# Kernel tuning notes

Measured on AMD Instinct MI355X. Metric: run time of the kernel, lower is better.

The kernel has to match this reference:

```python
import jax, jax.numpy as jnp
import numpy as np

D_STATE = 8
DT_RANK = 16
D_CONV = 4


def layernorm(x, w, b, eps=1e-5):
    mu = jnp.mean(x, axis=-1, keepdims=True)
    var = jnp.var(x, axis=-1, keepdims=True)
    return (x - mu) * jax.lax.rsqrt(var + eps) * w + b


def silu(x):
    return x * jax.nn.sigmoid(x)


def dwconv_causal(x, w, b):
    # x: [B,L,D], w: [D,K] depthwise causal conv (mamba conv1d, padding=K-1 then truncate)
    K = w.shape[1]
    xp = jnp.pad(x, ((0, 0), (K - 1, 0), (0, 0)))
    y = jax.lax.conv_general_dilated(
        xp, w.T[:, None, :], (1,), 'VALID',
        dimension_numbers=('NWC', 'WIO', 'NWC'),
        feature_group_count=w.shape[0])
    return y + b


def selective_scan(u, dt, A, Bm, Cm, Dp):
    # u, dt: [b,l,d]; A: [d,n]; Bm, Cm: [b,l,n]; Dp: [d]
    def step(h, inp):
        dt_t, B_t, C_t, u_t = inp           # [b,d],[b,n],[b,n],[b,d]
        dA = jnp.exp(dt_t[..., None] * A)   # [b,d,n]
        h = dA * h + dt_t[..., None] * B_t[:, None, :] * u_t[..., None]
        y = jnp.einsum('bdn,bn->bd', h, C_t)
        return h, y
    b, l, d = u.shape
    h0 = jnp.zeros((b, d, A.shape[1]), u.dtype)
    xs = (dt.transpose(1, 0, 2), Bm.transpose(1, 0, 2),
          Cm.transpose(1, 0, 2), u.transpose(1, 0, 2))
    _, ys = jax.lax.scan(step, h0, xs)
    return ys.transpose(1, 0, 2) + u * Dp


def scan_dir(x, xe, cw, cb, cew, ceb, xpw, dtw, dtb, A_log, Dp):
    # one scan direction: u from x (input0 path), dt/B/C from xe (extra_emb path)
    xc = silu(dwconv_causal(x, cw, cb))
    ec = silu(dwconv_causal(xe, cew, ceb))
    dbl = ec @ xpw.T                                   # [b,l,dt_rank+2n]
    dtr = dbl[..., :DT_RANK]
    Bm = dbl[..., DT_RANK:DT_RANK + D_STATE]
    Cm = dbl[..., DT_RANK + D_STATE:]
    dt = jax.nn.softplus(dtr @ dtw.T + dtb)
    A = -jnp.exp(A_log)
    return selective_scan(xc, dt, A, Bm, Cm, Dp)


def forward(input0, input1, norm0_w, norm0_b, norm1_w, norm1_b,
            in_proj_w, in_proj_extra_w,
            convx_w, convx_b, conve_w, conve_b,
            convx_w_r, convx_b_r, conve_w_r, conve_b_r,
            xproj_w, xproj_w_r, dtproj_w, dtproj_b, dtproj_w_r, dtproj_b_r,
            A_log, A_log_r, Dp, Dp_r, outnorm_w, outnorm_b, outproj_w):
    skip = input0
    h0 = layernorm(input0, norm0_w, norm0_b)
    h1 = layernorm(input1, norm1_w, norm1_b)
    xz = h0 @ in_proj_w.T                     # [b,l,2d]
    d = in_proj_w.shape[0] // 2
    x, z = xz[..., :d], xz[..., d:]
    xe = h1 @ in_proj_extra_w.T               # [b,l,d]
    # forward-direction scan
    y_f = scan_dir(x, xe, convx_w, convx_b, conve_w, conve_b,
                   xproj_w, dtproj_w, dtproj_b, A_log, Dp)
    # backward-direction scan (flip sequence, scan, flip back)
    xr, xer = jnp.flip(x, 1), jnp.flip(xe, 1)
    y_b = scan_dir(xr, xer, convx_w_r, convx_b_r, conve_w_r, conve_b_r,
                   xproj_w_r, dtproj_w_r, dtproj_b_r, A_log_r, Dp_r)
    y = (y_f + jnp.flip(y_b, 1)) * 0.5        # if_devide_out=True
    y = layernorm(y, outnorm_w, outnorm_b)    # use_norm=True
    y = y * silu(z)
    out = y @ outproj_w.T
    return out + skip


def setup_inputs() -> dict:
    key = jax.random.key(0)
    B, H, W, dim = 2, 128, 128, 256
    L, d, n, dtr, K = H * W, dim, D_STATE, DT_RANK, D_CONV
    ks = jax.random.split(key, 24)
    s = 0.02
    inp = {
        'input0': jax.random.normal(ks[0], (B, L, dim), jnp.float32),
        'input1': jax.random.normal(ks[1], (B, L, dim), jnp.float32),
        'norm0_w': jnp.ones((dim,), jnp.float32),
        'norm0_b': jnp.zeros((dim,), jnp.float32),
        'norm1_w': jnp.ones((dim,), jnp.float32),
        'norm1_b': jnp.zeros((dim,), jnp.float32),
        'in_proj_w': jax.random.normal(ks[2], (2 * d, dim), jnp.float32) * s,
        'in_proj_extra_w': jax.random.normal(ks[3], (d, dim), jnp.float32) * s,
        'convx_w': jax.random.normal(ks[4], (d, K), jnp.float32) * 0.2,
        'convx_b': jnp.zeros((d,), jnp.float32),
        'conve_w': jax.random.normal(ks[5], (d, K), jnp.float32) * 0.2,
        'conve_b': jnp.zeros((d,), jnp.float32),
        'convx_w_r': jax.random.normal(ks[6], (d, K), jnp.float32) * 0.2,
        'convx_b_r': jnp.zeros((d,), jnp.float32),
        'conve_w_r': jax.random.normal(ks[7], (d, K), jnp.float32) * 0.2,
        'conve_b_r': jnp.zeros((d,), jnp.float32),
        'xproj_w': jax.random.normal(ks[8], (dtr + 2 * n, d), jnp.float32) * s,
        'xproj_w_r': jax.random.normal(ks[9], (dtr + 2 * n, d), jnp.float32) * s,
        'dtproj_w': jax.random.normal(ks[10], (d, dtr), jnp.float32) * 0.1,
        'dtproj_b': jax.random.uniform(ks[11], (d,), jnp.float32, -4.0, -2.0),
        'dtproj_w_r': jax.random.normal(ks[12], (d, dtr), jnp.float32) * 0.1,
        'dtproj_b_r': jax.random.uniform(ks[13], (d,), jnp.float32, -4.0, -2.0),
        'A_log': jnp.tile(jnp.log(jnp.arange(1, n + 1, dtype=jnp.float32)), (d, 1)),
        'A_log_r': jnp.tile(jnp.log(jnp.arange(1, n + 1, dtype=jnp.float32)), (d, 1)),
        'Dp': jnp.ones((d,), jnp.float32),
        'Dp_r': jnp.ones((d,), jnp.float32),
        'outnorm_w': jnp.ones((d,), jnp.float32),
        'outnorm_b': jnp.zeros((d,), jnp.float32),
        'outproj_w': jax.random.normal(ks[14], (dim, d), jnp.float32) * s,
    }
    return inp


def reference(input0, input1, norm0_w, norm0_b, norm1_w, norm1_b,
              in_proj_w, in_proj_extra_w,
              convx_w, convx_b, conve_w, conve_b,
              convx_w_r, convx_b_r, conve_w_r, conve_b_r,
              xproj_w, xproj_w_r, dtproj_w, dtproj_b, dtproj_w_r, dtproj_b_r,
              A_log, A_log_r, Dp, Dp_r, outnorm_w, outnorm_b, outproj_w):
    return forward(input0, input1, norm0_w, norm0_b, norm1_w, norm1_b,
                   in_proj_w, in_proj_extra_w,
                   convx_w, convx_b, conve_w, conve_b,
                   convx_w_r, convx_b_r, conve_w_r, conve_b_r,
                   xproj_w, xproj_w_r, dtproj_w, dtproj_b, dtproj_w_r, dtproj_b_r,
                   A_log, A_log_r, Dp, Dp_r, outnorm_w, outnorm_b, outproj_w)
```

## Files before the change

### kernel.cpp

```cpp
#include <hip/hip_runtime.h>
#include <math.h>

#define L_SEQ 16384
#define DIM 256
#define NST 8
#define RNK 16
#define S_TOT 32768
#define NCH 512
#define CLH 32

typedef __attribute__((ext_vector_type(8))) short bf16x8;
typedef __attribute__((ext_vector_type(4))) float f32x4;

__device__ __forceinline__ float bf2f(unsigned short u) {
  union { unsigned int i; float f; } v; v.i = ((unsigned int)u) << 16; return v.f;
}
__device__ __forceinline__ unsigned short f2bf(float x) {
  union { float f; unsigned int i; } v; v.f = x;
  unsigned int r = v.i + 0x7fffu + ((v.i >> 16) & 1u);
  return (unsigned short)(r >> 16);
}
__device__ __forceinline__ float rcpf(float x) {
  return __builtin_amdgcn_rcpf(x);
}

__global__ __launch_bounds__(256) void wconv(
    const float* __restrict__ w0, const float* __restrict__ w1,
    const float* __restrict__ w2, unsigned short* __restrict__ out) {
  int i = blockIdx.x * 256 + threadIdx.x;
  if (i < 131072) out[i] = f2bf(w0[i]);
  else if (i < 196608) out[i] = f2bf(w1[i - 131072]);
  else out[i] = f2bf(w2[i - 196608]);
}

__global__ __launch_bounds__(256) void ln_norm(
    const float* __restrict__ in0, const float* __restrict__ in1,
    const float* __restrict__ w0, const float* __restrict__ b0,
    const float* __restrict__ w1, const float* __restrict__ b1,
    unsigned short* __restrict__ h0, unsigned short* __restrict__ h1) {
  int which = blockIdx.y;
  int row = blockIdx.x * 4 + (threadIdx.x >> 6);
  int lane = threadIdx.x & 63;
  const float* x = (which ? in1 : in0) + (size_t)row * DIM;
  const float* w = which ? w1 : w0;
  const float* b = which ? b1 : b0;
  unsigned short* h = which ? h1 : h0;
  float4 v = *(const float4*)&x[lane * 4];
  float s = v.x + v.y + v.z + v.w;
  float s2 = v.x * v.x + v.y * v.y + v.z * v.z + v.w * v.w;
  for (int off = 32; off; off >>= 1) {
    s += __shfl_xor(s, off);
    s2 += __shfl_xor(s2, off);
  }
  float mean = s * (1.0f / DIM);
  float var = s2 * (1.0f / DIM) - mean * mean;
  float rstd = rsqrtf(var + 1e-5f);
  float4 wv = *(const float4*)&w[lane * 4];
  float4 bv = *(const float4*)&b[lane * 4];
  ushort4 out;
  out.x = f2bf((v.x - mean) * rstd * wv.x + bv.x);
  out.y = f2bf((v.y - mean) * rstd * wv.y + bv.y);
  out.z = f2bf((v.z - mean) * rstd * wv.z + bv.z);
  out.w = f2bf((v.w - mean) * rstd * wv.w + bv.w);
  *(ushort4*)&h[(size_t)row * DIM + lane * 4] = out;
}

template <int BF16C, int ADDIN>
__global__ __launch_bounds__(256) void gemm64(
    const unsigned short* __restrict__ A, int lda,
    const unsigned short* __restrict__ Wb,
    void* __restrict__ Cv, const float* __restrict__ addp, int Nn) {
  __shared__ unsigned short As[64 * 256];
  __shared__ unsigned short Ws[64 * 256];
  int tid = threadIdx.x;
  int n0 = blockIdx.x * 64, m0 = blockIdx.y * 64;
  for (int i = 0; i < 8; ++i) {
    int f8 = tid + i * 256;
    int r = f8 >> 5, c8 = (f8 & 31) * 8;
    int sc = c8 ^ ((r & 7) << 3);
    *(uint4*)&As[r * 256 + sc] = *(const uint4*)&A[(size_t)(m0 + r) * lda + c8];
    *(uint4*)&Ws[r * 256 + sc] = *(const uint4*)&Wb[(size_t)(n0 + r) * 256 + c8];
  }
  __syncthreads();
  int wid = tid >> 6, lane = tid & 63;
  int wm = wid >> 1, wn = wid & 1;
  int l15 = lane & 15, lk = (lane >> 4) * 8;
  f32x4 acc[2][2] = {};
  for (int ks = 0; ks < 8; ++ks) {
    int kcol = ks * 32 + lk;
    bf16x8 af[2], bf_[2];
    for (int mf = 0; mf < 2; ++mf) {
      int row = wm * 32 + mf * 16 + l15;
      af[mf] = *(const bf16x8*)&As[row * 256 + (kcol ^ ((row & 7) << 3))];
    }
    for (int nf = 0; nf < 2; ++nf) {
      int row = wn * 32 + nf * 16 + l15;
      bf_[nf] = *(const bf16x8*)&Ws[row * 256 + (kcol ^ ((row & 7) << 3))];
    }
    for (int mf = 0; mf < 2; ++mf)
      for (int nf = 0; nf < 2; ++nf)
        acc[mf][nf] = __builtin_amdgcn_mfma_f32_16x16x32_bf16(
            af[mf], bf_[nf], acc[mf][nf], 0, 0, 0);
  }
  for (int mf = 0; mf < 2; ++mf)
    for (int nf = 0; nf < 2; ++nf) {
      int row = m0 + wm * 32 + mf * 16 + (lane >> 4) * 4;
      int col = n0 + wn * 32 + nf * 16 + l15;
      for (int v = 0; v < 4; ++v) {
        size_t off = (size_t)(row + v) * Nn + col;
        float val = acc[mf][nf][v];
        if (ADDIN) val += addp[off];
        if (BF16C) ((unsigned short*)Cv)[off] = f2bf(val);
        else       ((float*)Cv)[off] = val;
      }
    }
}

__global__ __launch_bounds__(256) void xproj_mfma(
    const unsigned short* __restrict__ xe,
    const float* __restrict__ conve_w, const float* __restrict__ conve_b,
    const float* __restrict__ conve_w_r, const float* __restrict__ conve_b_r,
    const float* __restrict__ xproj_w, const float* __restrict__ xproj_w_r,
    float* __restrict__ dbl2) {
  __shared__ unsigned short ecS[64 * 256];
  __shared__ unsigned short xwS[32 * 256];
  int chunk = blockIdx.x;
  int dir = blockIdx.y;
  int b = chunk >> 8;
  int t0 = (chunk & 255) * 64;
  int tid = threadIdx.x;
  const float* cw = dir ? conve_w_r : conve_w;
  const float* cb = dir ? conve_b_r : conve_b;
  const float* xw = dir ? xproj_w_r : xproj_w;

  for (int i = tid; i < 32 * 256; i += 256) {
    int o = i >> 8, dd = i & 255;
    xwS[o * 256 + (((dd & ~7) ^ ((o & 7) << 3)) | (dd & 7))] = f2bf(xw[i]);
  }

  {
    int c = tid;
    float w0 = cw[c * 4 + 0], w1 = cw[c * 4 + 1], w2 = cw[c * 4 + 2],
          w3 = cw[c * 4 + 3], bias = cb[c];
    size_t bL = (size_t)b * L_SEQ;
    auto loadx = [&](int t) -> float {
      if (t < 0) return 0.f;
      int src = dir ? (L_SEQ - 1 - t) : t;
      return bf2f(xe[(bL + src) * DIM + c]);
    };
    float xm3 = loadx(t0 - 3), xm2 = loadx(t0 - 2), xm1 = loadx(t0 - 1);
    const unsigned short* xp =
        &xe[(bL + (dir ? (L_SEQ - 1 - t0) : t0)) * DIM + c];
    int xstep = dir ? -DIM : DIM;
    int cbase = c & ~7, clow = c & 7;
    for (int t4 = 0; t4 < 64; t4 += 4) {
      float xin4[4];
      for (int j = 0; j < 4; ++j) xin4[j] = bf2f(xp[(ptrdiff_t)j * xstep]);
      xp += (ptrdiff_t)4 * xstep;
      for (int j = 0; j < 4; ++j) {
        int tl = t4 + j;
        float xin = xin4[j];
        float pre = w0 * xm3 + w1 * xm2 + w2 * xm1 + w3 * xin + bias;
        float u = pre * rcpf(1.f + __expf(-pre));
        xm3 = xm2; xm2 = xm1; xm1 = xin;
        ecS[tl * 256 + ((cbase ^ ((tl & 7) << 3)) | clow)] = f2bf(u);
      }
    }
  }
  __syncthreads();

  int wid = tid >> 6, lane = tid & 63;
  int l15 = lane & 15, lk = (lane >> 4) * 8;
  f32x4 acc[2] = {};
  for (int kk = 0; kk < 8; ++kk) {
    int kcol = kk * 32 + lk;
    int row = wid * 16 + l15;
    bf16x8 af = *(const bf16x8*)&ecS[row * 256 + (kcol ^ ((row & 7) << 3))];
    for (int ni = 0; ni < 2; ++ni) {
      int o = ni * 16 + l15;
      bf16x8 bfr = *(const bf16x8*)&xwS[o * 256 + (kcol ^ ((o & 7) << 3))];
      acc[ni] = __builtin_amdgcn_mfma_f32_16x16x32_bf16(af, bfr, acc[ni], 0, 0, 0);
    }
  }
  size_t mbase = (size_t)dir * S_TOT + (size_t)chunk * 64;
  int rloc = wid * 16 + (lane >> 4) * 4;
  for (int ni = 0; ni < 2; ++ni) {
    int o = ni * 16 + l15;
    for (int v = 0; v < 4; ++v)
      dbl2[(mbase + rloc + v) * 32 + o] = acc[ni][v];
  }
}

__global__ __launch_bounds__(256) void dt_mfma(
    const float* __restrict__ dbl2,
    const float* __restrict__ dtw, const float* __restrict__ dtw_r,
    const float* __restrict__ dtb, const float* __restrict__ dtb_r,
    unsigned short* __restrict__ dt_arr) {
  __shared__ unsigned short dtwS[256 * 32];
  __shared__ unsigned short dtrS[64 * 32];
  __shared__ unsigned short outS[64 * 256];
  int m0 = blockIdx.x * 64;
  int dir = (blockIdx.x >= 512) ? 1 : 0;
  int tid = threadIdx.x;
  const float* dw = dir ? dtw_r : dtw;
  const float* db = dir ? dtb_r : dtb;
  {
    uint4 z; z.x = 0; z.y = 0; z.z = 0; z.w = 0;
    for (int i = tid; i < 1280; i += 256) {
      if (i < 1024) ((uint4*)dtwS)[i] = z;
      else          ((uint4*)dtrS)[i - 1024] = z;
    }
  }
  __syncthreads();
  for (int it = 0; it < 4; ++it) {
    int idx = tid + it * 256;
    int c = idx >> 2, k4 = idx & 3;
    float4 v = *(const float4*)&dw[c * 16 + k4 * 4];
    uint2 pk;
    pk.x = (unsigned int)f2bf(v.x) | ((unsigned int)f2bf(v.y) << 16);
    pk.y = (unsigned int)f2bf(v.z) | ((unsigned int)f2bf(v.w) << 16);
    int byte = c * 64 + (((k4 >> 1) ^ (c & 3)) << 4) + ((k4 & 1) << 3);
    *(uint2*)((char*)dtwS + byte) = pk;
  }
  {
    int r = tid >> 2, k4 = tid & 3;
    float4 v = *(const float4*)&dbl2[(size_t)(m0 + r) * 32 + k4 * 4];
    uint2 pk;
    pk.x = (unsigned int)f2bf(v.x) | ((unsigned int)f2bf(v.y) << 16);
    pk.y = (unsigned int)f2bf(v.z) | ((unsigned int)f2bf(v.w) << 16);
    int byte = r * 64 + (((k4 >> 1) ^ (r & 3)) << 4) + ((k4 & 1) << 3);
    *(uint2*)((char*)dtrS + byte) = pk;
  }
  __syncthreads();
  int wid = tid >> 6, lane = tid & 63;
  int l15 = lane & 15, lkc = lane >> 4;
  bf16x8 af[4];
  for (int mi = 0; mi < 4; ++mi) {
    int r = mi * 16 + l15;
    af[mi] = *(const bf16x8*)((char*)dtrS + r * 64 + ((lkc ^ (r & 3)) << 4));
  }
  f32x4 acc[4][4] = {};
  for (int ni = 0; ni < 4; ++ni) {
    int c = (wid * 4 + ni) * 16 + l15;
    bf16x8 bfr = *(const bf16x8*)((char*)dtwS + c * 64 + ((lkc ^ (c & 3)) << 4));
    for (int mi = 0; mi < 4; ++mi)
      acc[mi][ni] = __builtin_amdgcn_mfma_f32_16x16x32_bf16(
          af[mi], bfr, acc[mi][ni], 0, 0, 0);
  }
  for (int ni = 0; ni < 4; ++ni) {
    int c = (wid * 4 + ni) * 16 + l15;
    float bias_ = db[c];
    int cb_ = c & ~7, cl_ = c & 7;
    for (int mi = 0; mi < 4; ++mi) {
      int rb = mi * 16 + (lane >> 4) * 4;
      for (int v = 0; v < 4; ++v) {
        int r = rb + v;
        float xdt = acc[mi][ni][v] + bias_;
        float dtv = (xdt > 15.f) ? xdt : __logf(1.f + __expf(xdt));
        outS[r * 256 + ((cb_ ^ ((r & 7) << 3)) | cl_)] = f2bf(dtv);
      }
    }
  }
  __syncthreads();
  for (int it = 0; it < 8; ++it) {
    int i = tid + it * 256;
    int r = i >> 5, cg = (i & 31) * 8;
    uint4 val = *(const uint4*)&outS[r * 256 + (cg ^ ((r & 7) << 3))];
    *(uint4*)&dt_arr[(size_t)(m0 + r) * 256 + cg] = val;
  }
}

__global__ __launch_bounds__(256) void u_compute(
    const unsigned short* __restrict__ xz,
    const float* __restrict__ convx_w, const float* __restrict__ convx_b,
    const float* __restrict__ convx_w_r, const float* __restrict__ convx_b_r,
    unsigned short* __restrict__ u_arr) {
  int chunk = blockIdx.x;
  int dir = blockIdx.y;
  int b = chunk >> 9;
  int t0 = (chunk & 511) * 32;
  int c = threadIdx.x;
  const float* cw = dir ? convx_w_r : convx_w;
  const float* cb = dir ? convx_b_r : convx_b;
  float w0 = cw[c * 4 + 0], w1 = cw[c * 4 + 1], w2 = cw[c * 4 + 2],
        w3 = cw[c * 4 + 3], bias = cb[c];
  size_t dtbase = (size_t)dir * S_TOT + (size_t)b * L_SEQ;
  size_t bL = (size_t)b * L_SEQ;
  float xm3, xm2, xm1;
  {
    auto loadx = [&](int t) -> float {
      if (t < 0) return 0.f;
      int src = dir ? (L_SEQ - 1 - t) : t;
      return bf2f(xz[(bL + src) * 512 + c]);
    };
    xm3 = loadx(t0 - 3); xm2 = loadx(t0 - 2); xm1 = loadx(t0 - 1);
  }
  const unsigned short* xp = &xz[(bL + (dir ? (L_SEQ - 1 - t0) : t0)) * 512 + c];
  ptrdiff_t xstep = dir ? -512 : 512;
  unsigned short* op = &u_arr[(dtbase + t0) * DIM + c];
  for (int t4 = 0; t4 < 32; t4 += 4) {
    float xin4[4];
    for (int j = 0; j < 4; ++j) xin4[j] = bf2f(xp[(ptrdiff_t)j * xstep]);
    xp += 4 * xstep;
    for (int j = 0; j < 4; ++j) {
      float xin = xin4[j];
      float pre = w0 * xm3 + w1 * xm2 + w2 * xm1 + w3 * xin + bias;
      float u = pre * rcpf(1.f + __expf(-pre));
      xm3 = xm2; xm2 = xm1; xm1 = xin;
      op[(size_t)j * DIM] = f2bf(u);
    }
    op += 4 * DIM;
  }
}

#define DA8(FASTA)                                                    \
  float dA[NST];                                                      \
  if (FASTA) {                                                        \
    float e1 = __expf(-dtv);                                          \
    dA[0] = e1;                                                       \
    for (int n = 1; n < NST; ++n) dA[n] = dA[n - 1] * e1;             \
  } else {                                                            \
    for (int n = 0; n < NST; ++n) dA[n] = __expf(dtv * Ar[n]);        \
  }

template <int USE_UDT>
__global__ __launch_bounds__(256) void scan_pass1(
    const unsigned short* __restrict__ xz, const float* __restrict__ dbl2,
    const unsigned short* __restrict__ u_arr,
    const unsigned short* __restrict__ dt_arr,
    const float* __restrict__ convx_w, const float* __restrict__ convx_b,
    const float* __restrict__ convx_w_r, const float* __restrict__ convx_b_r,
    const float* __restrict__ dtproj_w, const float* __restrict__ dtproj_b,
    const float* __restrict__ dtproj_w_r, const float* __restrict__ dtproj_b_r,
    const float* __restrict__ A_log, const float* __restrict__ A_log_r,
    float* __restrict__ Pc, float* __restrict__ Qc) {
  int chunk = blockIdx.x, b = blockIdx.y, dir = blockIdx.z;
  int d = threadIdx.x;
  const float* al = dir ? A_log_r : A_log;
  float w0 = 0.f, w1 = 0.f, w2 = 0.f, w3 = 0.f, bias = 0.f, dbias = 0.f;
  float dwreg[RNK];
  if (!USE_UDT) {
    const float* cw = dir ? convx_w_r : convx_w;
    const float* cb = dir ? convx_b_r : convx_b;
    const float* dw = dir ? dtproj_w_r : dtproj_w;
    const float* dbp = dir ? dtproj_b_r : dtproj_b;
    w0 = cw[d * 4 + 0]; w1 = cw[d * 4 + 1]; w2 = cw[d * 4 + 2];
    w3 = cw[d * 4 + 3]; bias = cb[d]; dbias = dbp[d];
    for (int r = 0; r < RNK; ++r) dwreg[r] = dw[d * RNK + r];
  }
  float Ar[NST];
  bool fa = true;
  for (int n = 0; n < NST; ++n) {
    Ar[n] = -__expf(al[d * NST + n]);
    fa = fa && (fabsf(Ar[n] + (float)(n + 1)) < 1e-4f * (float)(n + 1));
  }
  bool fastA = (__ballot(fa) == ~0ULL);

  __shared__ float dblS[CLH][32];
  int t0 = chunk * CLH;
  size_t dtbase = (size_t)dir * S_TOT + (size_t)b * L_SEQ;
  if (USE_UDT) {
    int i = d;
    dblS[i >> 3][i & 7] = dbl2[(dtbase + t0 + (i >> 3)) * 32 + 16 + (i & 7)];
  } else {
    for (int i = d; i < CLH * 32; i += 256)
      dblS[i >> 5][i & 31] = dbl2[(dtbase + t0) * 32 + i];
  }
  __syncthreads();
  auto loadx = [&](int t) -> float {
    if (t < 0) return 0.f;
    int srct = dir ? (L_SEQ - 1 - t) : t;
    return bf2f(xz[((size_t)b * L_SEQ + srct) * 512 + d]);
  };
  float xm3 = 0.f, xm2 = 0.f, xm1 = 0.f;
  if (!USE_UDT) { xm3 = loadx(t0 - 3); xm2 = loadx(t0 - 2); xm1 = loadx(t0 - 1); }
  const unsigned short* up = &u_arr[(dtbase + t0) * DIM + d];
  const unsigned short* dtp = &dt_arr[(dtbase + t0) * DIM + d];
  float Q[NST];
  for (int n = 0; n < NST; ++n) Q[n] = 0.f;
  float sdt = 0.f;
  const int BOFF = USE_UDT ? 0 : 16;

#define P1_GRP(FASTA)                                                      \
  for (int t8 = 0; t8 < CLH; t8 += 8) {                                    \
    float uu[8], dd[8];                                                    \
    for (int j = 0; j < 8; ++j) {                                          \
      uu[j] = bf2f(up[(size_t)j * DIM]);                                   \
      dd[j] = bf2f(dtp[(size_t)j * DIM]);                                  \
    }                                                                      \
    up += 8 * DIM; dtp += 8 * DIM;                                         \
    for (int j = 0; j < 8; ++j) {                                          \
      const float* row = dblS[t8 + j];                                     \
      float u = uu[j], dtv = dd[j];                                        \
      float du = dtv * u;                                                  \
      sdt += dtv;                                                          \
      DA8(FASTA)                                                           \
      float4 B0 = *(const float4*)(row);                                   \
      float4 B1 = *(const float4*)(row + 4);                               \
      Q[0] = dA[0] * Q[0] + du * B0.x; Q[1] = dA[1] * Q[1] + du * B0.y;    \
      Q[2] = dA[2] * Q[2] + du * B0.z; Q[3] = dA[3] * Q[3] + du * B0.w;    \
      Q[4] = dA[4] * Q[4] + du * B1.x; Q[5] = dA[5] * Q[5] + du * B1.y;    \
      Q[6] = dA[6] * Q[6] + du * B1.z; Q[7] = dA[7] * Q[7] + du * B1.w;    \
    }                                                                      \
  }

#define P1_STEP(FASTA)                                                     \
  {                                                                        \
    const float* row = dblS[tl];                                           \
    float u, dtv;                                                          \
    {                                                                      \
      float xin = loadx(t0 + tl);                                          \
      float pre = w0 * xm3 + w1 * xm2 + w2 * xm1 + w3 * xin + bias;        \
      u = pre * rcpf(1.f + __expf(-pre));                                  \
      xm3 = xm2; xm2 = xm1; xm1 = xin;                                     \
      float4 q0 = *(const float4*)(row);                                   \
      float4 q1 = *(const float4*)(row + 4);                               \
      float4 q2 = *(const float4*)(row + 8);                               \
      float4 q3 = *(const float4*)(row + 12);                              \
      float xdt = dbias + q0.x * dwreg[0] + q0.y * dwreg[1] +              \
                  q0.z * dwreg[2] + q0.w * dwreg[3] + q1.x * dwreg[4] +    \
                  q1.y * dwreg[5] + q1.z * dwreg[6] + q1.w * dwreg[7] +    \
                  q2.x * dwreg[8] + q2.y * dwreg[9] + q2.z * dwreg[10] +   \
                  q2.w * dwreg[11] + q3.x * dwreg[12] + q3.y * dwreg[13] + \
                  q3.z * dwreg[14] + q3.w * dwreg[15];                     \
      dtv = (xdt > 15.f) ? xdt : __logf(1.f + __expf(xdt));                \
    }                                                                      \
    float du = dtv * u;                                                    \
    sdt += dtv;                                                            \
    DA8(FASTA)                                                             \
    float4 B0 = *(const float4*)(row + BOFF);                              \
    float4 B1 = *(const float4*)(row + BOFF + 4);                          \
    Q[0] = dA[0] * Q[0] + du * B0.x; Q[1] = dA[1] * Q[1] + du * B0.y;      \
    Q[2] = dA[2] * Q[2] + du * B0.z; Q[3] = dA[3] * Q[3] + du * B0.w;      \
    Q[4] = dA[4] * Q[4] + du * B1.x; Q[5] = dA[5] * Q[5] + du * B1.y;      \
    Q[6] = dA[6] * Q[6] + du * B1.z; Q[7] = dA[7] * Q[7] + du * B1.w;      \
  }

  if (USE_UDT) {
    if (fastA) { P1_GRP(1) } else { P1_GRP(0) }
  } else {
    if (fastA) {
      for (int tl = 0; tl < CLH; ++tl) P1_STEP(1)
    } else {
      for (int tl = 0; tl < CLH; ++tl) P1_STEP(0)
    }
  }
#undef P1_STEP
#undef P1_GRP

  float P[NST];
  if (fastA) {
    float E = __expf(-sdt);
    P[0] = E;
    for (int n = 1; n < NST; ++n) P[n] = P[n - 1] * E;
  } else {
    for (int n = 0; n < NST; ++n) P[n] = __expf(Ar[n] * sdt);
  }
  size_t obase = ((((size_t)(dir * 2 + b)) * NCH + chunk) * DIM + d) * NST;
  for (int n = 0; n < NST; ++n) { Pc[obase + n] = P[n]; Qc[obase + n] = Q[n]; }
}

__global__ __launch_bounds__(256) void scan_mid(
    float* __restrict__ Pc, const float* __restrict__ Qc) {
  int idx = blockIdx.x * 256 + threadIdx.x;
  int dn = idx & 2047;
  int db_ = idx >> 11;
  size_t base = (size_t)db_ * NCH * 2048 + dn;
  float h = 0.f;
  for (int c0 = 0; c0 < NCH; c0 += 8) {
    size_t off = base + (size_t)c0 * 2048;
    float P[8], Q[8];
#pragma unroll
    for (int j = 0; j < 8; ++j) {
      P[j] = Pc[off + (size_t)j * 2048];
      Q[j] = Qc[off + (size_t)j * 2048];
    }
#pragma unroll
    for (int j = 0; j < 8; ++j) {
      Pc[off + (size_t)j * 2048] = h;
      h = P[j] * h + Q[j];
    }
  }
}

template <int MODE>
__global__ __launch_bounds__(256) void scan_pass2(
    const unsigned short* __restrict__ xz, const float* __restrict__ dbl2,
    unsigned short* __restrict__ u_arr,
    const unsigned short* __restrict__ dt_arr,
    const float* __restrict__ convx_w, const float* __restrict__ convx_b,
    const float* __restrict__ convx_w_r, const float* __restrict__ convx_b_r,
    const float* __restrict__ dtproj_w, const float* __restrict__ dtproj_b,
    const float* __restrict__ dtproj_w_r, const float* __restrict__ dtproj_b_r,
    const float* __restrict__ A_log, const float* __restrict__ A_log_r,
    const float* __restrict__ Dp, const float* __restrict__ Dp_r,
    const float* __restrict__ Hinit, unsigned short* __restrict__ ycomb,
    int dirParam) {
  int chunk = blockIdx.x, b = blockIdx.y;
  int dir = MODE ? blockIdx.z : dirParam;
  int d = threadIdx.x;
  const float* al = dir ? A_log_r : A_log;
  float Dv = (dir ? Dp_r : Dp)[d];
  float w0 = 0.f, w1 = 0.f, w2 = 0.f, w3 = 0.f, bias = 0.f, dbias = 0.f;
  float dwreg[RNK];
  if (!MODE) {
    const float* cw = dir ? convx_w_r : convx_w;
    const float* cb = dir ? convx_b_r : convx_b;
    const float* dw = dir ? dtproj_w_r : dtproj_w;
    const float* dbp = dir ? dtproj_b_r : dtproj_b;
    w0 = cw[d * 4 + 0]; w1 = cw[d * 4 + 1]; w2 = cw[d * 4 + 2];
    w3 = cw[d * 4 + 3]; bias = cb[d];
    dbias = dbp[d];
    for (int r = 0; r < RNK; ++r) dwreg[r] = dw[d * RNK + r];
  }
  float Ar[NST];
  bool fa = true;
  for (int n = 0; n < NST; ++n) {
    Ar[n] = -__expf(al[d * NST + n]);
    fa = fa && (fabsf(Ar[n] + (float)(n + 1)) < 1e-4f * (float)(n + 1));
  }
  bool fastA = (__ballot(fa) == ~0ULL);

  __shared__ float dblS[CLH][32];
  int t0 = chunk * CLH;
  size_t dtbase = (size_t)dir * S_TOT + (size_t)b * L_SEQ;
  if (MODE) {
    for (int i = d; i < CLH * 16; i += 256)
      dblS[i >> 4][i & 15] = dbl2[(dtbase + t0 + (i >> 4)) * 32 + 16 + (i & 15)];
  } else {
    for (int i = d; i < CLH * 32; i += 256)
      dblS[i >> 5][i & 31] = dbl2[(dtbase + t0) * 32 + i];
  }
  __syncthreads();
  auto loadx = [&](int t) -> float {
    if (t < 0) return 0.f;
    int srct = dir ? (L_SEQ - 1 - t) : t;
    return bf2f(xz[((size_t)b * L_SEQ + srct) * 512 + d]);
  };
  float xm3 = 0.f, xm2 = 0.f, xm1 = 0.f;
  if (!MODE) { xm3 = loadx(t0 - 3); xm2 = loadx(t0 - 2); xm1 = loadx(t0 - 1); }
  float h[NST];
  size_t hbase = ((((size_t)(dir * 2 + b)) * NCH + chunk) * DIM + d) * NST;
  for (int n = 0; n < NST; ++n) h[n] = Hinit[hbase + n];
  unsigned short* up = &u_arr[(dtbase + t0) * DIM + d];
  const unsigned short* dtp = &dt_arr[(dtbase + t0) * DIM + d];
  unsigned short* yc = &ycomb[((size_t)b * L_SEQ + t0) * DIM + d];

#define P2_GRP(FASTA)                                                      \
  for (int t8 = 0; t8 < CLH; t8 += 8) {                                    \
    float uu[8], dd[8];                                                    \
    for (int j = 0; j < 8; ++j) {                                          \
      uu[j] = bf2f(up[(size_t)j * DIM]);                                   \
      dd[j] = bf2f(dtp[(size_t)j * DIM]);                                  \
    }                                                                      \
    for (int j = 0; j < 8; ++j) {                                          \
      const float* row = dblS[t8 + j];                                     \
      float u = uu[j], dtv = dd[j];                                        \
      float du = dtv * u;                                                  \
      DA8(FASTA)                                                           \
      float4 B0 = *(const float4*)(row);                                   \
      float4 B1 = *(const float4*)(row + 4);                               \
      float4 C0 = *(const float4*)(row + 8);                               \
      float4 C1 = *(const float4*)(row + 12);                              \
      h[0] = dA[0] * h[0] + du * B0.x; h[1] = dA[1] * h[1] + du * B0.y;    \
      h[2] = dA[2] * h[2] + du * B0.z; h[3] = dA[3] * h[3] + du * B0.w;    \
      h[4] = dA[4] * h[4] + du * B1.x; h[5] = dA[5] * h[5] + du * B1.y;    \
      h[6] = dA[6] * h[6] + du * B1.z; h[7] = dA[7] * h[7] + du * B1.w;    \
      float y = C0.x * h[0] + C0.y * h[1] + C0.z * h[2] + C0.w * h[3] +    \
                C1.x * h[4] + C1.y * h[5] + C1.z * h[6] + C1.w * h[7] +    \
                u * Dv;                                                    \
      if (dir == 0) yc[(size_t)j * DIM] = f2bf(y);                         \
      else          up[(size_t)j * DIM] = f2bf(y);                         \
    }                                                                      \
    up += 8 * DIM; dtp += 8 * DIM; yc += 8 * DIM;                          \
  }

#define P2_STEP(FASTA)                                                     \
  {                                                                        \
    int t = t0 + tl;                                                       \
    const float* row = dblS[tl];                                           \
    float u, dtv;                                                          \
    {                                                                      \
      float xin = loadx(t);                                                \
      float pre = w0 * xm3 + w1 * xm2 + w2 * xm1 + w3 * xin + bias;        \
      u = pre * rcpf(1.f + __expf(-pre));                                  \
      xm3 = xm2; xm2 = xm1; xm1 = xin;                                     \
      float4 q0 = *(const float4*)(row);                                   \
      float4 q1 = *(const float4*)(row + 4);                               \
      float4 q2 = *(const float4*)(row + 8);                               \
      float4 q3 = *(const float4*)(row + 12);                              \
      float xdt = dbias + q0.x * dwreg[0] + q0.y * dwreg[1] +              \
                  q0.z * dwreg[2] + q0.w * dwreg[3] + q1.x * dwreg[4] +    \
                  q1.y * dwreg[5] + q1.z * dwreg[6] + q1.w * dwreg[7] +    \
                  q2.x * dwreg[8] + q2.y * dwreg[9] + q2.z * dwreg[10] +   \
                  q2.w * dwreg[11] + q3.x * dwreg[12] + q3.y * dwreg[13] + \
                  q3.z * dwreg[14] + q3.w * dwreg[15];                     \
      dtv = (xdt > 15.f) ? xdt : __logf(1.f + __expf(xdt));                \
    }                                                                      \
    float du = dtv * u;                                                    \
    DA8(FASTA)                                                             \
    float4 B0 = *(const float4*)(row + 16);                                \
    float4 B1 = *(const float4*)(row + 20);                                \
    float4 C0 = *(const float4*)(row + 24);                                \
    float4 C1 = *(const float4*)(row + 28);                                \
    h[0] = dA[0] * h[0] + du * B0.x; h[1] = dA[1] * h[1] + du * B0.y;      \
    h[2] = dA[2] * h[2] + du * B0.z; h[3] = dA[3] * h[3] + du * B0.w;      \
    h[4] = dA[4] * h[4] + du * B1.x; h[5] = dA[5] * h[5] + du * B1.y;      \
    h[6] = dA[6] * h[6] + du * B1.z; h[7] = dA[7] * h[7] + du * B1.w;      \
    float y = C0.x * h[0] + C0.y * h[1] + C0.z * h[2] + C0.w * h[3] +      \
              C1.x * h[4] + C1.y * h[5] + C1.z * h[6] + C1.w * h[7] +      \
              u * Dv;                                                      \
    if (dir == 0) {                                                        \
      ycomb[((size_t)b * L_SEQ + t) * DIM + d] = f2bf(y);                  \
    } else {                                                               \
      size_t o = ((size_t)b * L_SEQ + (L_SEQ - 1 - t)) * DIM + d;          \
      float prev = bf2f(ycomb[o]);                                         \
      ycomb[o] = f2bf(0.5f * (prev + y));                                  \
    }                                                                      \
  }

  if (MODE) {
    if (fastA) { P2_GRP(1) } else { P2_GRP(0) }
  } else {
    if (fastA) {
      for (int tl = 0; tl < CLH; ++tl) P2_STEP(1)
    } else {
      for (int tl = 0; tl < CLH; ++tl) P2_STEP(0)
    }
  }
#undef P2_STEP
#undef P2_GRP
}

template <int MERGED>
__global__ __launch_bounds__(256) void combine_ln(
    const unsigned short* __restrict__ ycomb,
    const unsigned short* __restrict__ ybu,
    unsigned short* __restrict__ xz,
    const float* __restrict__ onw, const float* __restrict__ onb) {
  int m = blockIdx.x * 4 + (threadIdx.x >> 6);
  int lane = threadIdx.x & 63;
  ushort4 y4 = *(const ushort4*)&ycomb[(size_t)m * DIM + lane * 4];
  float v0 = bf2f(y4.x), v1 = bf2f(y4.y), v2 = bf2f(y4.z), v3 = bf2f(y4.w);
  if (MERGED) {
    int b = m >> 14, l = m & (L_SEQ - 1);
    size_t fo = ((size_t)S_TOT + (size_t)b * L_SEQ + (L_SEQ - 1 - l)) * DIM +
                lane * 4;
    ushort4 yb4 = *(const ushort4*)&ybu[fo];
    v0 = 0.5f * (v0 + bf2f(yb4.x)); v1 = 0.5f * (v1 + bf2f(yb4.y));
    v2 = 0.5f * (v2 + bf2f(yb4.z)); v3 = 0.5f * (v3 + bf2f(yb4.w));
  }
  float s = v0 + v1 + v2 + v3;
  float s2 = v0 * v0 + v1 * v1 + v2 * v2 + v3 * v3;
  for (int off = 32; off; off >>= 1) {
    s += __shfl_xor(s, off);
    s2 += __shfl_xor(s2, off);
  }
  float mean = s * (1.0f / DIM);
  float var = s2 * (1.0f / DIM) - mean * mean;
  float rstd = rsqrtf(var + 1e-5f);
  ushort4 z4 = *(const ushort4*)&xz[(size_t)m * 512 + 256 + lane * 4];
  float zf[4] = {bf2f(z4.x), bf2f(z4.y), bf2f(z4.z), bf2f(z4.w)};
  float vf[4] = {v0, v1, v2, v3};
  ushort4 out;
  unsigned short* op = (unsigned short*)&out;
  for (int j = 0; j < 4; ++j) {
    int c = lane * 4 + j;
    float ln = (vf[j] - mean) * rstd * onw[c] + onb[c];
    op[j] = f2bf(ln * (zf[j] * rcpf(1.f + __expf(-zf[j]))));
  }
  *(ushort4*)&xz[(size_t)m * 512 + lane * 4] = out;
}

extern "C" void kernel_launch(void* const* d_in, const int* in_sizes, int n_in,
                              void* d_out, int out_size, void* d_ws, size_t ws_size,
                              hipStream_t stream) {
  const float* input0 = (const float*)d_in[0];
  const float* input1 = (const float*)d_in[1];
  const float* norm0_w = (const float*)d_in[2];
  const float* norm0_b = (const float*)d_in[3];
  const float* norm1_w = (const float*)d_in[4];
  const float* norm1_b = (const float*)d_in[5];
  const float* in_proj_w = (const float*)d_in[6];
  const float* in_proj_extra_w = (const float*)d_in[7];
  const float* convx_w = (const float*)d_in[8];
  const float* convx_b = (const float*)d_in[9];
  const float* conve_w = (const float*)d_in[10];
  const float* conve_b = (const float*)d_in[11];
  const float* convx_w_r = (const float*)d_in[12];
  const float* convx_b_r = (const float*)d_in[13];
  const float* conve_w_r = (const float*)d_in[14];
  const float* conve_b_r = (const float*)d_in[15];
  const float* xproj_w = (const float*)d_in[16];
  const float* xproj_w_r = (const float*)d_in[17];
  const float* dtproj_w = (const float*)d_in[18];
  const float* dtproj_b = (const float*)d_in[19];
  const float* dtproj_w_r = (const float*)d_in[20];
  const float* dtproj_b_r = (const float*)d_in[21];
  const float* A_log = (const float*)d_in[22];
  const float* A_log_r = (const float*)d_in[23];
  const float* Dp = (const float*)d_in[24];
  const float* Dp_r = (const float*)d_in[25];
  const float* outnorm_w = (const float*)d_in[26];
  const float* outnorm_b = (const float*)d_in[27];
  const float* outproj_w = (const float*)d_in[28];

  char* w = (char*)d_ws;
  unsigned short* xz    = (unsigned short*)(w + 0);
  unsigned short* h1    = (unsigned short*)(w + 0);
  unsigned short* h0    = (unsigned short*)(w + 33554432);
  unsigned short* ycomb = (unsigned short*)(w + 33554432);
  float* Qc   = (float*)(w + 33554432);
  unsigned short* xe    = (unsigned short*)(w + 50331648);
  float* Pc   = (float*)(w + 50331648);
  float* dbl2 = (float*)(w + 67108864);
  unsigned short* wb = (unsigned short*)(w + 75497472);
  unsigned short* wb_in  = wb;
  unsigned short* wb_ex  = wb + 131072;
  unsigned short* wb_out = wb + 196608;
  unsigned short* u_arr  = (unsigned short*)(w + 76021760);
  unsigned short* dt_arr = (unsigned short*)(w + 109576192);
  const bool big = ws_size >= 76021760ULL + 67108864ULL;

  wconv<<<dim3(1024), 256, 0, stream>>>(in_proj_w, in_proj_extra_w, outproj_w, wb);
  ln_norm<<<dim3(S_TOT / 4, 2), 256, 0, stream>>>(
      input0, input1, norm0_w, norm0_b, norm1_w, norm1_b, h0, h1);
  gemm64<1, 0><<<dim3(4, 512), 256, 0, stream>>>(h1, DIM, wb_ex, xe, nullptr, 256);
  gemm64<1, 0><<<dim3(8, 512), 256, 0, stream>>>(h0, DIM, wb_in, xz, nullptr, 512);
  xproj_mfma<<<dim3(512, 2), 256, 0, stream>>>(
      xe, conve_w, conve_b, conve_w_r, conve_b_r, xproj_w, xproj_w_r, dbl2);
  if (big) {
    dt_mfma<<<dim3(1024), 256, 0, stream>>>(
        dbl2, dtproj_w, dtproj_w_r, dtproj_b, dtproj_b_r, dt_arr);
    u_compute<<<dim3(1024, 2), 256, 0, stream>>>(
        xz, convx_w, convx_b, convx_w_r, convx_b_r, u_arr);
    scan_pass1<1><<<dim3(NCH, 2, 2), 256, 0, stream>>>(
        xz, dbl2, u_arr, dt_arr, convx_w, convx_b, convx_w_r, convx_b_r,
        dtproj_w, dtproj_b, dtproj_w_r, dtproj_b_r, A_log, A_log_r, Pc, Qc);
  } else {
    scan_pass1<0><<<dim3(NCH, 2, 2), 256, 0, stream>>>(
        xz, dbl2, u_arr, dt_arr, convx_w, convx_b, convx_w_r, convx_b_r,
        dtproj_w, dtproj_b, dtproj_w_r, dtproj_b_r, A_log, A_log_r, Pc, Qc);
  }
  scan_mid<<<dim3(32), 256, 0, stream>>>(Pc, Qc);
  if (big) {
    scan_pass2<1><<<dim3(NCH, 2, 2), 256, 0, stream>>>(
        xz, dbl2, u_arr, dt_arr, convx_w, convx_b, convx_w_r, convx_b_r,
        dtproj_w, dtproj_b, dtproj_w_r, dtproj_b_r, A_log, A_log_r,
        Dp, Dp_r, Pc, ycomb, 0);
    combine_ln<1><<<dim3(S_TOT / 4), 256, 0, stream>>>(
        ycomb, u_arr, xz, outnorm_w, outnorm_b);
  } else {
    for (int dir = 0; dir < 2; ++dir)
      scan_pass2<0><<<dim3(NCH, 2), 256, 0, stream>>>(
          xz, dbl2, u_arr, dt_arr, convx_w, convx_b, convx_w_r, convx_b_r,
          dtproj_w, dtproj_b, dtproj_w_r, dtproj_b_r, A_log, A_log_r,
          Dp, Dp_r, Pc, ycomb, dir);
    combine_ln<0><<<dim3(S_TOT / 4), 256, 0, stream>>>(
        ycomb, nullptr, xz, outnorm_w, outnorm_b);
  }
  gemm64<0, 1><<<dim3(4, 512), 256, 0, stream>>>(
      xz, 512, wb_out, d_out, input0, 256);
}
```

Before: 230.0 us.

## Store x-projection output as bf16 and compute both conv directions per u_compute block

```diff
diff --git a/kernel.cpp b/kernel.cpp
--- a/kernel.cpp
+++ b/kernel.cpp
@@ -121,7 +121,7 @@
     const float* __restrict__ conve_w, const float* __restrict__ conve_b,
     const float* __restrict__ conve_w_r, const float* __restrict__ conve_b_r,
     const float* __restrict__ xproj_w, const float* __restrict__ xproj_w_r,
-    float* __restrict__ dbl2) {
+    unsigned short* __restrict__ dbl2) {
   __shared__ unsigned short ecS[64 * 256];
   __shared__ unsigned short xwS[32 * 256];
   int chunk = blockIdx.x;
@@ -187,12 +187,12 @@
   for (int ni = 0; ni < 2; ++ni) {
     int o = ni * 16 + l15;
     for (int v = 0; v < 4; ++v)
-      dbl2[(mbase + rloc + v) * 32 + o] = acc[ni][v];
+      dbl2[(mbase + rloc + v) * 32 + o] = f2bf(acc[ni][v]);
   }
 }
 
 __global__ __launch_bounds__(256) void dt_mfma(
-    const float* __restrict__ dbl2,
+    const unsigned short* __restrict__ dbl2,
     const float* __restrict__ dtw, const float* __restrict__ dtw_r,
     const float* __restrict__ dtb, const float* __restrict__ dtb_r,
     unsigned short* __restrict__ dt_arr) {
@@ -224,10 +224,7 @@
   }
   {
     int r = tid >> 2, k4 = tid & 3;
-    float4 v = *(const float4*)&dbl2[(size_t)(m0 + r) * 32 + k4 * 4];
-    uint2 pk;
-    pk.x = (unsigned int)f2bf(v.x) | ((unsigned int)f2bf(v.y) << 16);
-    pk.y = (unsigned int)f2bf(v.z) | ((unsigned int)f2bf(v.w) << 16);
+    uint2 pk = *(const uint2*)&dbl2[(size_t)(m0 + r) * 32 + k4 * 4];
     int byte = r * 64 + (((k4 >> 1) ^ (r & 3)) << 4) + ((k4 & 1) << 3);
     *(uint2*)((char*)dtrS + byte) = pk;
   }
@@ -276,40 +273,40 @@
     const float* __restrict__ convx_w_r, const float* __restrict__ convx_b_r,
     unsigned short* __restrict__ u_arr) {
   int chunk = blockIdx.x;
-  int dir = blockIdx.y;
   int b = chunk >> 9;
   int t0 = (chunk & 511) * 32;
   int c = threadIdx.x;
-  const float* cw = dir ? convx_w_r : convx_w;
-  const float* cb = dir ? convx_b_r : convx_b;
-  float w0 = cw[c * 4 + 0], w1 = cw[c * 4 + 1], w2 = cw[c * 4 + 2],
-        w3 = cw[c * 4 + 3], bias = cb[c];
-  size_t dtbase = (size_t)dir * S_TOT + (size_t)b * L_SEQ;
+  float w0 = convx_w[c * 4 + 0], w1 = convx_w[c * 4 + 1],
+        w2 = convx_w[c * 4 + 2], w3 = convx_w[c * 4 + 3], bias = convx_b[c];
+  float w0r = convx_w_r[c * 4 + 0], w1r = convx_w_r[c * 4 + 1],
+        w2r = convx_w_r[c * 4 + 2], w3r = convx_w_r[c * 4 + 3],
+        biasr = convx_b_r[c];
   size_t bL = (size_t)b * L_SEQ;
-  float xm3, xm2, xm1;
-  {
-    auto loadx = [&](int t) -> float {
-      if (t < 0) return 0.f;
-      int src = dir ? (L_SEQ - 1 - t) : t;
-      return bf2f(xz[(bL + src) * 512 + c]);
-    };
-    xm3 = loadx(t0 - 3); xm2 = loadx(t0 - 2); xm1 = loadx(t0 - 1);
-  }
-  const unsigned short* xp = &xz[(bL + (dir ? (L_SEQ - 1 - t0) : t0)) * 512 + c];
-  ptrdiff_t xstep = dir ? -512 : 512;
-  unsigned short* op = &u_arr[(dtbase + t0) * DIM + c];
-  for (int t4 = 0; t4 < 32; t4 += 4) {
+  auto ld = [&](int t) -> float {
+    if (t < 0 || t >= L_SEQ) return 0.f;
+    return bf2f(xz[(bL + t) * 512 + c]);
+  };
+  float x3 = ld(t0 - 3), x2 = ld(t0 - 2), x1 = ld(t0 - 1);
+  unsigned short* op0 = &u_arr[(bL + t0) * DIM + c];
+  unsigned short* op1 =
+      &u_arr[((size_t)S_TOT + bL + (L_SEQ - 1 - t0)) * DIM + c];
+  for (int tg = 0; tg < 36; tg += 4) {
     float xin4[4];
-    for (int j = 0; j < 4; ++j) xin4[j] = bf2f(xp[(ptrdiff_t)j * xstep]);
-    xp += 4 * xstep;
+    for (int j = 0; j < 4; ++j) xin4[j] = ld(t0 + tg + j);
     for (int j = 0; j < 4; ++j) {
+      int tl = tg + j;
       float xin = xin4[j];
-      float pre = w0 * xm3 + w1 * xm2 + w2 * xm1 + w3 * xin + bias;
-      float u = pre * rcpf(1.f + __expf(-pre));
-      xm3 = xm2; xm2 = xm1; xm1 = xin;
-      op[(size_t)j * DIM] = f2bf(u);
-    }
-    op += 4 * DIM;
+      if (tl < 32) {
+        float pre = w0 * x3 + w1 * x2 + w2 * x1 + w3 * xin + bias;
+        op0[(size_t)tl * DIM] = f2bf(pre * rcpf(1.f + __expf(-pre)));
+      }
+      if (tl >= 3 && tl < 35) {
+        float prer = w0r * xin + w1r * x1 + w2r * x2 + w3r * x3 + biasr;
+        int s = tl - 3;
+        *(op1 - (ptrdiff_t)s * DIM) = f2bf(prer * rcpf(1.f + __expf(-prer)));
+      }
+      x3 = x2; x2 = x1; x1 = xin;
+    }
   }
 }
 
@@ -325,7 +322,7 @@
 
 template <int USE_UDT>
 __global__ __launch_bounds__(256) void scan_pass1(
-    const unsigned short* __restrict__ xz, const float* __restrict__ dbl2,
+    const unsigned short* __restrict__ xz, const unsigned short* __restrict__ dbl2,
     const unsigned short* __restrict__ u_arr,
     const unsigned short* __restrict__ dt_arr,
     const float* __restrict__ convx_w, const float* __restrict__ convx_b,
@@ -361,10 +358,11 @@
   size_t dtbase = (size_t)dir * S_TOT + (size_t)b * L_SEQ;
   if (USE_UDT) {
     int i = d;
-    dblS[i >> 3][i & 7] = dbl2[(dtbase + t0 + (i >> 3)) * 32 + 16 + (i & 7)];
+    dblS[i >> 3][i & 7] =
+        bf2f(dbl2[(dtbase + t0 + (i >> 3)) * 32 + 16 + (i & 7)]);
   } else {
     for (int i = d; i < CLH * 32; i += 256)
-      dblS[i >> 5][i & 31] = dbl2[(dtbase + t0) * 32 + i];
+      dblS[i >> 5][i & 31] = bf2f(dbl2[(dtbase + t0) * 32 + i]);
   }
   __syncthreads();
   auto loadx = [&](int t) -> float {
@@ -485,7 +483,7 @@
 
 template <int MODE>
 __global__ __launch_bounds__(256) void scan_pass2(
-    const unsigned short* __restrict__ xz, const float* __restrict__ dbl2,
+    const unsigned short* __restrict__ xz, const unsigned short* __restrict__ dbl2,
     unsigned short* __restrict__ u_arr,
     const unsigned short* __restrict__ dt_arr,
     const float* __restrict__ convx_w, const float* __restrict__ convx_b,
@@ -526,10 +524,11 @@
   size_t dtbase = (size_t)dir * S_TOT + (size_t)b * L_SEQ;
   if (MODE) {
     for (int i = d; i < CLH * 16; i += 256)
-      dblS[i >> 4][i & 15] = dbl2[(dtbase + t0 + (i >> 4)) * 32 + 16 + (i & 15)];
+      dblS[i >> 4][i & 15] =
+          bf2f(dbl2[(dtbase + t0 + (i >> 4)) * 32 + 16 + (i & 15)]);
   } else {
     for (int i = d; i < CLH * 32; i += 256)
-      dblS[i >> 5][i & 31] = dbl2[(dtbase + t0) * 32 + i];
+      dblS[i >> 5][i & 31] = bf2f(dbl2[(dtbase + t0) * 32 + i]);
   }
   __syncthreads();
   auto loadx = [&](int t) -> float {
@@ -713,7 +712,7 @@
   float* Qc   = (float*)(w + 33554432);
   unsigned short* xe    = (unsigned short*)(w + 50331648);
   float* Pc   = (float*)(w + 50331648);
-  float* dbl2 = (float*)(w + 67108864);
+  unsigned short* dbl2 = (unsigned short*)(w + 67108864);
   unsigned short* wb = (unsigned short*)(w + 75497472);
   unsigned short* wb_in  = wb;
   unsigned short* wb_ex  = wb + 131072;
@@ -732,7 +731,7 @@
   if (big) {
     dt_mfma<<<dim3(1024), 256, 0, stream>>>(
         dbl2, dtproj_w, dtproj_w_r, dtproj_b, dtproj_b_r, dt_arr);
-    u_compute<<<dim3(1024, 2), 256, 0, stream>>>(
+    u_compute<<<dim3(1024), 256, 0, stream>>>(
         xz, convx_w, convx_b, convx_w_r, convx_b_r, u_arr);
     scan_pass1<1><<<dim3(NCH, 2, 2), 256, 0, stream>>>(
         xz, dbl2, u_arr, dt_arr, convx_w, convx_b, convx_w_r, convx_b_r,
```

Measured after the change: 227.1 us. No clear change (-1.2%).
